# Optimization experiments

Measured on AMD Instinct MI355X. Metric: run time of the kernel, lower is better.

The kernel has to match this reference:

```python
import jax, jax.numpy as jnp
import numpy as np

NUM_CLASSES = 91
COST_CLASS, COST_BBOX, COST_GIOU = 1.0, 5.0, 2.0
W_CE, W_BBOX, W_GIOU = 2.0, 2.5, 2.0
EOS_COEF = 0.1
B, Q, T = 64, 300, 25


def box_cxcywh_to_xyxy(x):
    cx, cy, w, h = x[..., 0], x[..., 1], x[..., 2], x[..., 3]
    return jnp.stack([cx - 0.5 * w, cy - 0.5 * h, cx + 0.5 * w, cy + 0.5 * h], axis=-1)


def giou_pairwise(b1, b2):
    # b1 [N,4], b2 [M,4] in xyxy -> [N,M]
    area1 = (b1[:, 2] - b1[:, 0]) * (b1[:, 3] - b1[:, 1])
    area2 = (b2[:, 2] - b2[:, 0]) * (b2[:, 3] - b2[:, 1])
    lt = jnp.maximum(b1[:, None, :2], b2[None, :, :2])
    rb = jnp.minimum(b1[:, None, 2:], b2[None, :, 2:])
    wh = jnp.clip(rb - lt, 0.0)
    inter = wh[..., 0] * wh[..., 1]
    union = area1[:, None] + area2[None, :] - inter
    iou = inter / union
    lti = jnp.minimum(b1[:, None, :2], b2[None, :, :2])
    rbi = jnp.maximum(b1[:, None, 2:], b2[None, :, 2:])
    whi = jnp.clip(rbi - lti, 0.0)
    areai = whi[..., 0] * whi[..., 1]
    return iou - (areai - union) / areai


def giou_elementwise(b1, b2):
    # b1,b2 [N,4] xyxy -> [N]
    area1 = (b1[:, 2] - b1[:, 0]) * (b1[:, 3] - b1[:, 1])
    area2 = (b2[:, 2] - b2[:, 0]) * (b2[:, 3] - b2[:, 1])
    lt = jnp.maximum(b1[:, :2], b2[:, :2])
    rb = jnp.minimum(b1[:, 2:], b2[:, 2:])
    wh = jnp.clip(rb - lt, 0.0)
    inter = wh[:, 0] * wh[:, 1]
    union = area1 + area2 - inter
    iou = inter / union
    lti = jnp.minimum(b1[:, :2], b2[:, :2])
    rbi = jnp.maximum(b1[:, 2:], b2[:, 2:])
    whi = jnp.clip(rbi - lti, 0.0)
    areai = whi[:, 0] * whi[:, 1]
    return iou - (areai - union) / areai


def _lsa(cost):
    # Jonker-Volgenant shortest augmenting path; same optimum as scipy linear_sum_assignment
    cost = np.asarray(cost, dtype=np.float64)
    transposed = cost.shape[0] > cost.shape[1]
    if transposed:
        cost = cost.T
    n, m = cost.shape  # n <= m
    u = np.zeros(n + 1)
    v = np.zeros(m + 1)
    p = np.zeros(m + 1, dtype=np.int64)
    way = np.zeros(m + 1, dtype=np.int64)
    for i in range(1, n + 1):
        p[0] = i
        j0 = 0
        minv = np.full(m + 1, np.inf)
        used = np.zeros(m + 1, dtype=bool)
        while True:
            used[j0] = True
            i0 = p[j0]
            cur = cost[i0 - 1, :] - u[i0] - v[1:]
            free = ~used[1:]
            better = free & (cur < minv[1:])
            minv[1:][better] = cur[better]
            way[1:][better] = j0
            masked = np.where(free, minv[1:], np.inf)
            j1 = int(np.argmin(masked)) + 1
            delta = minv[j1]
            u[p[used]] += delta
            v[used] -= delta
            minv[~used] -= delta
            j0 = j1
            if p[j0] == 0:
                break
        while j0:
            j1 = way[j0]
            p[j0] = p[j1]
            j0 = j1
    rows, cols = [], []
    for j in range(1, m + 1):
        if p[j] != 0:
            rows.append(p[j] - 1)
            cols.append(j - 1)
    rows = np.asarray(rows, dtype=np.int64)
    cols = np.asarray(cols, dtype=np.int64)
    if transposed:
        rows, cols = cols, rows
    order = np.argsort(rows)
    return rows[order], cols[order]


def _match(pred_logits, pred_boxes, tgt_labels, tgt_boxes):
    # builds the full cross-batch cost matrix exactly like the torch module, then
    # solves per-image rectangular assignment on the host (non-differentiable)
    log_prob = jax.nn.log_softmax(pred_logits.reshape(B * Q, NUM_CLASSES + 1), axis=-1)
    out_bbox = pred_boxes.reshape(B * Q, 4)
    tgt_ids = tgt_labels.reshape(B * T)
    tgt_bb = tgt_boxes.reshape(B * T, 4)
    cost_class = -log_prob[:, tgt_ids]                                        # [BQ, BT]
    cost_bbox = jnp.abs(out_bbox[:, None, :] - tgt_bb[None, :, :]).sum(-1)    # L1 cdist
    cost_giou = -giou_pairwise(box_cxcywh_to_xyxy(out_bbox), box_cxcywh_to_xyxy(tgt_bb))
    C = COST_BBOX * cost_bbox + COST_CLASS * cost_class + COST_GIOU * cost_giou
    Cn = np.asarray(jax.lax.stop_gradient(C.reshape(B, Q, B * T)))
    src = np.zeros((B, T), dtype=np.int64)
    tgt = np.zeros((B, T), dtype=np.int64)
    for b in range(B):
        r, c = _lsa(Cn[b, :, b * T:(b + 1) * T])
        src[b] = r
        tgt[b] = c
    batch_idx = jnp.repeat(jnp.arange(B), T)
    return batch_idx, jnp.asarray(src.reshape(-1)), jnp.asarray(tgt.reshape(-1))


def _losses(pred_logits, pred_boxes, tgt_labels, tgt_boxes, batch_idx, src_idx, tgt_idx):
    num_t = batch_idx.shape[0]
    matched_labels = tgt_labels[batch_idx, tgt_idx]
    target_classes = jnp.full((B, Q), NUM_CLASSES, dtype=jnp.int32)
    target_classes = target_classes.at[batch_idx, src_idx].set(matched_labels)
    empty_weight = jnp.ones(NUM_CLASSES + 1, dtype=pred_logits.dtype).at[-1].set(EOS_COEF)
    logp = jax.nn.log_softmax(pred_logits, axis=-1)
    nll = -jnp.take_along_axis(logp, target_classes[..., None], axis=-1)[..., 0]
    w = empty_weight[target_classes]
    loss_ce = (w * nll).sum() / w.sum()
    src_b = pred_boxes[batch_idx, src_idx]
    tgt_b = tgt_boxes[batch_idx, tgt_idx]
    loss_bbox = jnp.abs(src_b - tgt_b).sum() / num_t
    loss_giou = (1.0 - giou_elementwise(box_cxcywh_to_xyxy(src_b), box_cxcywh_to_xyxy(tgt_b))).sum() / num_t
    l_ce = W_CE * loss_ce
    l_bb = W_BBOX * loss_bbox
    l_gi = W_GIOU * loss_giou
    return jnp.stack([l_ce, l_bb, l_gi, l_ce + l_bb + l_gi])


def setup_inputs() -> dict:
    key = jax.random.key(0)
    k1, k2, k3, k4 = jax.random.split(key, 4)
    pred_logits = jax.random.normal(k1, (B, Q, NUM_CLASSES + 1), dtype=jnp.float32)
    pred_boxes = jax.random.uniform(k2, (B, Q, 4), dtype=jnp.float32, minval=0.05, maxval=0.95)
    tgt_labels = jax.random.randint(k3, (B, T), 0, NUM_CLASSES)
    tgt_boxes = jax.random.uniform(k4, (B, T, 4), dtype=jnp.float32, minval=0.05, maxval=0.95)
    return {"pred_logits": pred_logits, "pred_boxes": pred_boxes, "tgt_labels": tgt_labels, "tgt_boxes": tgt_boxes}


def reference(pred_logits, pred_boxes, tgt_labels, tgt_boxes):
    batch_idx, src_idx, tgt_idx = _match(pred_logits, pred_boxes, tgt_labels, tgt_boxes)
    # returns [loss_ce, loss_bbox, loss_giou, loss_total] (already weight-scaled)
    return _losses(pred_logits, pred_boxes, tgt_labels, tgt_boxes, batch_idx, src_idx, tgt_idx)
```

## Files before the change

### kernel.cpp

```cpp
#include <hip/hip_runtime.h>
#include <math.h>

constexpr int B_ = 64;
constexpr int Q_ = 300;
constexpr int T_ = 25;
constexpr int NCLS = 91;
constexpr int L_ = NCLS + 1;
constexpr float C_BB = 5.0f, C_GI = 2.0f;
constexpr float W_CE = 2.0f, W_BBOX = 2.5f, W_GIOU = 2.0f;
constexpr float EOS = 0.1f;
constexpr int K_ = 5;
constexpr int TPB = 256;

__device__ __forceinline__ unsigned long long ord64(double v) {
    long long bb = __double_as_longlong(v);
    return (bb < 0) ? ~(unsigned long long)bb
                    : ((unsigned long long)bb | 0x8000000000000000ULL);
}
__device__ __forceinline__ double unord64(unsigned long long u) {
    long long bb = (u & 0x8000000000000000ULL) ? (long long)(u & 0x7FFFFFFFFFFFFFFFULL)
                                               : (long long)~u;
    return __longlong_as_double(bb);
}
__device__ __forceinline__ unsigned int ord32(float f) {
    unsigned int b = __float_as_uint(f);
    return (b & 0x80000000u) ? ~b : (b | 0x80000000u);
}
__device__ __forceinline__ unsigned long long pack14(double v, unsigned aux) {
    return (ord64(v) & ~16383ULL) | (unsigned long long)aux;
}
__device__ __forceinline__ unsigned long long pack9(double v, unsigned col) {
    return (ord64(v) & ~511ULL) | (unsigned long long)col;
}

template <int CTRL>
__device__ __forceinline__ unsigned long long dppb(unsigned long long b) {
    int lo = __builtin_amdgcn_update_dpp(0, (int)(unsigned)b, CTRL, 0xF, 0xF, true);
    int hi = __builtin_amdgcn_update_dpp(0, (int)(unsigned)(b >> 32), CTRL, 0xF, 0xF, true);
    return ((unsigned long long)(unsigned)hi << 32) | (unsigned)lo;
}
__device__ __forceinline__ unsigned long long bcast63(unsigned long long b) {
    unsigned lo = (unsigned)__builtin_amdgcn_readlane((int)(unsigned)b, 63);
    unsigned hi = (unsigned)__builtin_amdgcn_readlane((int)(unsigned)(b >> 32), 63);
    return ((unsigned long long)hi << 32) | lo;
}
__device__ __forceinline__ double readlane_f64(double v, int lane) {
    long long b = __double_as_longlong(v);
    int lo = __builtin_amdgcn_readlane((int)(unsigned)(unsigned long long)b, lane);
    int hi = __builtin_amdgcn_readlane((int)(((unsigned long long)b) >> 32), lane);
    return __longlong_as_double((long long)(((unsigned long long)(unsigned)hi << 32)
                                           | (unsigned)lo));
}

__device__ __forceinline__ unsigned long long wavemin(unsigned long long b) {
    { unsigned long long o = dppb<0xB1>(b);  if (o < b) b = o; }
    { unsigned long long o = dppb<0x4E>(b);  if (o < b) b = o; }
    { unsigned long long o = dppb<0x141>(b); if (o < b) b = o; }
    { unsigned long long o = dppb<0x140>(b); if (o < b) b = o; }
    { unsigned long long o = dppb<0x142>(b); if (o < b) b = o; }
    { unsigned long long o = dppb<0x143>(b); if (o < b) b = o; }
    return bcast63(b);
}
__device__ __forceinline__ void red2(unsigned long long& k1, unsigned long long& k2,
                                     unsigned long long o1, unsigned long long o2) {
    unsigned long long n1 = o1 < k1 ? o1 : k1;
    unsigned long long ls = o1 < k1 ? k1 : o1;
    unsigned long long n2 = k2 < o2 ? k2 : o2;
    n2 = ls < n2 ? ls : n2;
    k1 = n1; k2 = n2;
}
__device__ __forceinline__ void wavemin2(unsigned long long& k1, unsigned long long& k2) {
    red2(k1, k2, dppb<0xB1>(k1),  dppb<0xB1>(k2));
    red2(k1, k2, dppb<0x4E>(k1),  dppb<0x4E>(k2));
    red2(k1, k2, dppb<0x141>(k1), dppb<0x141>(k2));
    red2(k1, k2, dppb<0x140>(k1), dppb<0x140>(k2));
    red2(k1, k2, dppb<0x142>(k1), dppb<0x142>(k2));
    red2(k1, k2, dppb<0x143>(k1), dppb<0x143>(k2));
    k1 = bcast63(k1);
    k2 = bcast63(k2);
}

__device__ __forceinline__ float giou_f(const float px[4], float parea,
                                        const float tx[4], float tarea) {
    float ltx = fmaxf(px[0], tx[0]), lty = fmaxf(px[1], tx[1]);
    float rbx = fminf(px[2], tx[2]), rby = fminf(px[3], tx[3]);
    float iw = fmaxf(rbx - ltx, 0.f), ih = fmaxf(rby - lty, 0.f);
    float inter = iw * ih;
    float uni = parea + tarea - inter;
    float iou = inter / uni;
    float lix = fminf(px[0], tx[0]), liy = fminf(px[1], tx[1]);
    float rix = fmaxf(px[2], tx[2]), riy = fmaxf(px[3], tx[3]);
    float aw = fmaxf(rix - lix, 0.f), ah = fmaxf(riy - liy, 0.f);
    float ai = aw * ah;
    return iou - (ai - uni) / ai;
}

__global__ __launch_bounds__(TPB) void fused_kernel(
        const float* __restrict__ logits,
        const float* __restrict__ pboxes,
        const int*   __restrict__ tlabels,
        const float* __restrict__ tboxes,
        double* __restrict__ partial) {
    const int b = blockIdx.x;
    const int tid = threadIdx.x;

    __shared__ float  costL[T_][Q_];
    __shared__ float  lseL[Q_];
    __shared__ int    pL[Q_ + 1];
    __shared__ int    wayL[Q_ + 1];
    __shared__ double uL[T_ + 1];
    __shared__ double uStage[32];
    __shared__ int    argcolL[T_];
    __shared__ int    mqL[T_];
    __shared__ int    lblL[T_];
    __shared__ int    lblq[Q_];
    __shared__ float  tbL[T_][4];
    __shared__ float  txL[T_][4];
    __shared__ float  taL[T_];
    __shared__ double wsum[4][3];

    if (tid < T_) {
        lblL[tid] = tlabels[b * T_ + tid];
        mqL[tid] = 0;
        float c0 = tboxes[(size_t)(b * T_ + tid) * 4 + 0];
        float c1 = tboxes[(size_t)(b * T_ + tid) * 4 + 1];
        float c2 = tboxes[(size_t)(b * T_ + tid) * 4 + 2];
        float c3 = tboxes[(size_t)(b * T_ + tid) * 4 + 3];
        tbL[tid][0] = c0; tbL[tid][1] = c1; tbL[tid][2] = c2; tbL[tid][3] = c3;
        float x0 = c0 - 0.5f * c2, y0 = c1 - 0.5f * c3;
        float x1 = c0 + 0.5f * c2, y1 = c1 + 0.5f * c3;
        txL[tid][0] = x0; txL[tid][1] = y0; txL[tid][2] = x1; txL[tid][3] = y1;
        taL[tid] = (x1 - x0) * (y1 - y0);
    }
    for (int j = tid; j <= Q_; j += TPB) { pL[j] = 0; wayL[j] = 0; }
    for (int q = tid; q < Q_; q += TPB) lblq[q] = NCLS;
    __syncthreads();

    const float* lgb = logits + (size_t)b * Q_ * L_;
    const float* pbb = pboxes + (size_t)b * Q_ * 4;

    for (int q = tid; q < Q_; q += TPB) {
        const float4* lr4 = (const float4*)(lgb + (size_t)q * L_);
        float m0 = -INFINITY, m1 = -INFINITY, m2 = -INFINITY, m3 = -INFINITY;
        for (int c = 0; c < 23; ++c) {
            float4 v = lr4[c];
            m0 = fmaxf(m0, v.x); m1 = fmaxf(m1, v.y);
            m2 = fmaxf(m2, v.z); m3 = fmaxf(m3, v.w);
        }
        float mx = fmaxf(fmaxf(m0, m1), fmaxf(m2, m3));
        float s0 = 0.f, s1 = 0.f, s2 = 0.f, s3 = 0.f;
        for (int c = 0; c < 23; ++c) {
            float4 v = lr4[c];
            s0 += expf(v.x - mx); s1 += expf(v.y - mx);
            s2 += expf(v.z - mx); s3 += expf(v.w - mx);
        }
        float lz = mx + logf((s0 + s1) + (s2 + s3));
        lseL[q] = lz;

        float p0 = pbb[(size_t)q * 4 + 0], p1 = pbb[(size_t)q * 4 + 1];
        float p2 = pbb[(size_t)q * 4 + 2], p3 = pbb[(size_t)q * 4 + 3];
        float px[4] = { p0 - 0.5f * p2, p1 - 0.5f * p3, p0 + 0.5f * p2, p1 + 0.5f * p3 };
        float parea = (px[2] - px[0]) * (px[3] - px[1]);

#pragma unroll
        for (int t = 0; t < T_; ++t) {
            float cls = lz - lgb[(size_t)q * L_ + lblL[t]];
            float l1 = fabsf(p0 - tbL[t][0]) + fabsf(p1 - tbL[t][1]) +
                       fabsf(p2 - tbL[t][2]) + fabsf(p3 - tbL[t][3]);
            float tx[4] = { txL[t][0], txL[t][1], txL[t][2], txL[t][3] };
            float g = giou_f(px, parea, tx, taL[t]);
            costL[t][q] = C_BB * l1 + cls - C_GI * g;
        }
    }
    __syncthreads();

    {
        int w = tid >> 6, lane = tid & 63;
        for (int t = w; t < T_; t += 4) {
            unsigned long long best = ~0ULL;
#pragma unroll
            for (int k = 0; k < K_; ++k) {
                int col = lane + 64 * k;
                if (col < Q_) {
                    unsigned long long kk =
                        ((unsigned long long)ord32(costL[t][col]) << 32) | (unsigned)col;
                    if (kk < best) best = kk;
                }
            }
            best = wavemin(best);
            if (lane == 0) {
                int jc = (int)(best & 0xFFFFFFFFULL);
                argcolL[t] = jc;
                uL[t + 1] = (double)costL[t][jc];
            }
        }
    }
    __syncthreads();

    if (tid < 64) {
        int win = tid;
        if (tid < T_) {
            int myc = argcolL[tid];
            for (int j = 0; j < T_; ++j) {
                int oc = argcolL[j];
                if (oc == myc && j < win) win = j;
            }
            if (win == tid) pL[myc + 1] = tid + 1;
        }
        unsigned long long mb = __ballot(tid < T_ && win == tid);
        unsigned int freemask = (~(unsigned int)mb) & ((1u << T_) - 1);

        double v0[K_], minv[K_], stampv[K_];
        int pReg[K_];
        bool usedk[K_], validk[K_];
        double ureg = (tid >= 1 && tid <= T_) ? uL[tid] : 0.0;
#pragma unroll
        for (int k = 0; k < K_; ++k) {
            int col = tid + 64 * k;
            validk[k] = col < Q_;
            v0[k] = 0.0;
            stampv[k] = 0.0; usedk[k] = false; minv[k] = INFINITY;
            pReg[k] = validk[k] ? pL[col + 1] : 0;
        }

        for (int iter = 0; iter < 48 && freemask; ++iter) {
            int t = __builtin_ctz(freemask);
            freemask &= freemask - 1;
            const float* crow = &costL[t][0];
            unsigned long long k1 = ~0ULL, k2 = ~0ULL;
#pragma unroll
            for (int k = 0; k < K_; ++k) {
                if (validk[k]) {
                    int col = tid + 64 * k;
                    unsigned long long kk = pack9((double)crow[col] - v0[k], (unsigned)col);
                    if (kk < k1) { k2 = k1; k1 = kk; }
                    else if (kk < k2) { k2 = kk; }
                }
            }
            wavemin2(k1, k2);
            int j1 = (int)(k1 & 511ULL);
            double am1 = unord64(k1 & ~511ULL);
            double am2 = unord64(k2 & ~511ULL);
            int owner = j1 & 63, k1i = j1 >> 6;
            int psel = pReg[0];
#pragma unroll
            for (int k = 1; k < K_; ++k)
                if (k1i == k) psel = pReg[k];
            int prev = __builtin_amdgcn_readlane(psel, owner);
            if (tid == owner) {
#pragma unroll
                for (int k = 0; k < K_; ++k)
                    if (k == k1i) { v0[k] -= (am2 - am1); pReg[k] = t + 1; }
            }
            if (tid == t + 1) ureg = am2;
            if (prev) freemask |= 1u << (prev - 1);
        }

#pragma unroll
        for (int k = 0; k < K_; ++k)
            if (validk[k]) pL[tid + 1 + 64 * k] = pReg[k];

        for (int i = 1; i <= T_; ++i) {
            if (!((freemask >> (i - 1)) & 1u)) continue;
            if (tid == 0) pL[0] = i;
#pragma unroll
            for (int k = 0; k < K_; ++k) { minv[k] = INFINITY; usedk[k] = false; }
            double S = 0.0;
            int j0 = 0, i0 = i;
            double u0i0 = readlane_f64(ureg, i);

            for (int step = 0; step < 512; ++step) {
                double a = u0i0 - S;
                const float* crow = &costL[i0 - 1][0];
                unsigned long long bk = ~0ULL;
#pragma unroll
                for (int k = 0; k < K_; ++k) {
                    if (validk[k] && !usedk[k]) {
                        int col = tid + 64 * k;
                        double cur = (double)crow[col] - a - v0[k];
                        if (cur < minv[k]) { minv[k] = cur; wayL[col + 1] = j0; }
                        unsigned long long kk = pack14(
                            minv[k], ((unsigned)(col + 1) << 5) | (unsigned)pReg[k]);
                        if (kk < bk) bk = kk;
                    }
                }
                bk = wavemin(bk);
                int j1  = (int)((bk >> 5) & 511ULL);
                int i0n = (int)(bk & 31ULL);
                double Snew = unord64(bk & ~16383ULL);
                S = Snew;
                j0 = j1;
                if (i0n == 0) break;
                int owner = (j1 - 1) & 63, k1i = (j1 - 1) >> 6;
                if (tid == owner) {
#pragma unroll
                    for (int k = 0; k < K_; ++k)
                        if (k == k1i) { usedk[k] = true; stampv[k] = Snew; }
                }
                i0 = i0n;
                u0i0 = readlane_f64(ureg, i0);
            }

            if (tid <= T_) uStage[tid] = 0.0;
#pragma unroll
            for (int k = 0; k < K_; ++k) {
                if (validk[k] && usedk[k]) {
                    double d = S - stampv[k];
                    v0[k] -= d;
                    uStage[pReg[k]] = d;
                }
            }
            if (tid >= 1 && tid <= T_) ureg += uStage[tid];
            if (tid == i) ureg += S;
            if (tid == 0) {
                int jj = j0;
                while (jj) { int jn = wayL[jj]; pL[jj] = pL[jn]; jj = jn; }
            }
#pragma unroll
            for (int k = 0; k < K_; ++k)
                if (validk[k]) pReg[k] = pL[tid + 1 + 64 * k];
        }

#pragma unroll
        for (int k = 0; k < K_; ++k)
            if (validk[k] && pReg[k] > 0) mqL[pReg[k] - 1] = tid + 64 * k;
        if (tid < T_) lblq[mqL[tid]] = lblL[tid];
    }
    __syncthreads();

    double ce = 0.0, sb = 0.0, sg = 0.0;
    for (int q = tid; q < Q_; q += TPB) {
        int label = lblq[q];
        float nll = lseL[q] - lgb[(size_t)q * L_ + label];
        float w = (label == NCLS) ? EOS : 1.0f;
        ce += (double)(w * nll);
    }
    if (tid < T_) {
        int q = mqL[tid];
        float p0 = pbb[(size_t)q * 4 + 0], p1 = pbb[(size_t)q * 4 + 1];
        float p2 = pbb[(size_t)q * 4 + 2], p3 = pbb[(size_t)q * 4 + 3];
        sb = (double)(fabsf(p0 - tbL[tid][0]) + fabsf(p1 - tbL[tid][1]) +
                      fabsf(p2 - tbL[tid][2]) + fabsf(p3 - tbL[tid][3]));
        float px[4] = { p0 - 0.5f * p2, p1 - 0.5f * p3, p0 + 0.5f * p2, p1 + 0.5f * p3 };
        float parea = (px[2] - px[0]) * (px[3] - px[1]);
        float tx[4] = { txL[tid][0], txL[tid][1], txL[tid][2], txL[tid][3] };
        float g = giou_f(px, parea, tx, taL[tid]);
        sg = (double)(1.0f - g);
    }
#pragma unroll
    for (int off = 1; off < 64; off <<= 1) {
        ce += __shfl_xor(ce, off);
        sb += __shfl_xor(sb, off);
        sg += __shfl_xor(sg, off);
    }
    if ((tid & 63) == 0) {
        int w = tid >> 6;
        wsum[w][0] = ce; wsum[w][1] = sb; wsum[w][2] = sg;
    }
    __syncthreads();
    if (tid == 0) {
        double a0 = 0, a1 = 0, a2 = 0;
        for (int w = 0; w < 4; ++w) { a0 += wsum[w][0]; a1 += wsum[w][1]; a2 += wsum[w][2]; }
        partial[(size_t)b * 3 + 0] = a0;
        partial[(size_t)b * 3 + 1] = a1;
        partial[(size_t)b * 3 + 2] = a2;
    }
}

__global__ __launch_bounds__(64) void finalize_kernel(const double* __restrict__ partial,
                                                      float* __restrict__ out) {
    int tid = threadIdx.x;
    double a = partial[(size_t)tid * 3 + 0];
    double c = partial[(size_t)tid * 3 + 1];
    double g = partial[(size_t)tid * 3 + 2];
#pragma unroll
    for (int off = 1; off < 64; off <<= 1) {
        a += __shfl_xor(a, off);
        c += __shfl_xor(c, off);
        g += __shfl_xor(g, off);
    }
    if (tid == 0) {
        float lce = W_CE * (float)(a / 3360.0);
        float lbb = W_BBOX * (float)(c / 1600.0);
        float lgi = W_GIOU * (float)(g / 1600.0);
        out[0] = lce;
        out[1] = lbb;
        out[2] = lgi;
        out[3] = lce + lbb + lgi;
    }
}

extern "C" void kernel_launch(void* const* d_in, const int* in_sizes, int n_in,
                              void* d_out, int out_size, void* d_ws, size_t ws_size,
                              hipStream_t stream) {
    (void)in_sizes; (void)n_in; (void)out_size; (void)ws_size;
    const float* logits  = (const float*)d_in[0];
    const float* pboxes  = (const float*)d_in[1];
    const int*   tlabels = (const int*)d_in[2];
    const float* tboxes  = (const float*)d_in[3];
    float* out = (float*)d_out;
    double* partial = (double*)d_ws;

    fused_kernel<<<B_, TPB, 0, stream>>>(logits, pboxes, tlabels, tboxes, partial);
    finalize_kernel<<<1, 64, 0, stream>>>(partial, out);
}
```

Baseline: 36.47 us.

## Pair two free rows per auction step and fuse finalize via atomic last-block reduction

The auction-style initial assignment loop now processes two free target rows per iteration, scanning both cost rows together and running an interleaved double wave-min reduction. This is meant to halve the serial iteration count and hide reduction latency. On a column conflict the second row is returned to the free mask. Separately, the finalize kernel is replaced by atomic accumulation with a last-block counter, plus a memset. This trades a second kernel launch for a memset node and atomics, and makes the floating-point summation order nondeterministic.

```diff
diff --git a/kernel.cpp b/kernel.cpp
--- a/kernel.cpp
+++ b/kernel.cpp
@@ -78,6 +78,23 @@
     red2(k1, k2, dppb<0x143>(k1), dppb<0x143>(k2));
     k1 = bcast63(k1);
     k2 = bcast63(k2);
+}
+__device__ __forceinline__ void wavemin2x2(unsigned long long& a1, unsigned long long& a2,
+                                           unsigned long long& b1, unsigned long long& b2) {
+    red2(a1, a2, dppb<0xB1>(a1),  dppb<0xB1>(a2));
+    red2(b1, b2, dppb<0xB1>(b1),  dppb<0xB1>(b2));
+    red2(a1, a2, dppb<0x4E>(a1),  dppb<0x4E>(a2));
+    red2(b1, b2, dppb<0x4E>(b1),  dppb<0x4E>(b2));
+    red2(a1, a2, dppb<0x141>(a1), dppb<0x141>(a2));
+    red2(b1, b2, dppb<0x141>(b1), dppb<0x141>(b2));
+    red2(a1, a2, dppb<0x140>(a1), dppb<0x140>(a2));
+    red2(b1, b2, dppb<0x140>(b1), dppb<0x140>(b2));
+    red2(a1, a2, dppb<0x142>(a1), dppb<0x142>(a2));
+    red2(b1, b2, dppb<0x142>(b1), dppb<0x142>(b2));
+    red2(a1, a2, dppb<0x143>(a1), dppb<0x143>(a2));
+    red2(b1, b2, dppb<0x143>(b1), dppb<0x143>(b2));
+    a1 = bcast63(a1); a2 = bcast63(a2);
+    b1 = bcast63(b1); b2 = bcast63(b2);
 }
 
 __device__ __forceinline__ float giou_f(const float px[4], float parea,
@@ -100,7 +117,8 @@
         const float* __restrict__ pboxes,
         const int*   __restrict__ tlabels,
         const float* __restrict__ tboxes,
-        double* __restrict__ partial) {
+        double* acc,
+        float* out) {
     const int b = blockIdx.x;
     const int tid = threadIdx.x;
 
@@ -224,36 +242,68 @@
         }
 
         for (int iter = 0; iter < 48 && freemask; ++iter) {
-            int t = __builtin_ctz(freemask);
+            int t1 = __builtin_ctz(freemask);
             freemask &= freemask - 1;
-            const float* crow = &costL[t][0];
-            unsigned long long k1 = ~0ULL, k2 = ~0ULL;
+            int t2 = freemask ? __builtin_ctz(freemask) : -1;
+            if (t2 >= 0) freemask &= freemask - 1;
+
+            const float* crow1 = &costL[t1][0];
+            const float* crow2 = &costL[(t2 >= 0 ? t2 : t1)][0];
+            unsigned long long a1 = ~0ULL, a2 = ~0ULL, b1 = ~0ULL, b2 = ~0ULL;
 #pragma unroll
             for (int k = 0; k < K_; ++k) {
                 if (validk[k]) {
                     int col = tid + 64 * k;
-                    unsigned long long kk = pack9((double)crow[col] - v0[k], (unsigned)col);
-                    if (kk < k1) { k2 = k1; k1 = kk; }
-                    else if (kk < k2) { k2 = kk; }
-                }
-            }
-            wavemin2(k1, k2);
-            int j1 = (int)(k1 & 511ULL);
-            double am1 = unord64(k1 & ~511ULL);
-            double am2 = unord64(k2 & ~511ULL);
-            int owner = j1 & 63, k1i = j1 >> 6;
-            int psel = pReg[0];
-#pragma unroll
-            for (int k = 1; k < K_; ++k)
-                if (k1i == k) psel = pReg[k];
-            int prev = __builtin_amdgcn_readlane(psel, owner);
-            if (tid == owner) {
+                    double base = v0[k];
+                    unsigned long long ka = pack9((double)crow1[col] - base, (unsigned)col);
+                    if (ka < a1) { a2 = a1; a1 = ka; } else if (ka < a2) { a2 = ka; }
+                    unsigned long long kb = pack9((double)crow2[col] - base, (unsigned)col);
+                    if (kb < b1) { b2 = b1; b1 = kb; } else if (kb < b2) { b2 = kb; }
+                }
+            }
+            wavemin2x2(a1, a2, b1, b2);
+
+            int j1 = (int)(a1 & 511ULL);
+            double am1 = unord64(a1 & ~511ULL);
+            double am2 = unord64(a2 & ~511ULL);
+            int owner1 = j1 & 63, k1i = j1 >> 6;
+            int j2 = (t2 >= 0) ? (int)(b1 & 511ULL) : -1;
+            int owner2 = (j2 >= 0) ? (j2 & 63) : 0;
+            int k2i = (j2 >= 0) ? (j2 >> 6) : 0;
+
+            int psel1 = pReg[0], psel2 = pReg[0];
+#pragma unroll
+            for (int k = 1; k < K_; ++k) {
+                if (k1i == k) psel1 = pReg[k];
+                if (k2i == k) psel2 = pReg[k];
+            }
+            int prev1 = __builtin_amdgcn_readlane(psel1, owner1);
+            int prev2 = (j2 >= 0 && j2 != j1)
+                        ? __builtin_amdgcn_readlane(psel2, owner2) : 0;
+
+            if (tid == owner1) {
 #pragma unroll
                 for (int k = 0; k < K_; ++k)
-                    if (k == k1i) { v0[k] -= (am2 - am1); pReg[k] = t + 1; }
-            }
-            if (tid == t + 1) ureg = am2;
-            if (prev) freemask |= 1u << (prev - 1);
+                    if (k == k1i) { v0[k] -= (am2 - am1); pReg[k] = t1 + 1; }
+            }
+            if (tid == t1 + 1) ureg = am2;
+            if (prev1) freemask |= 1u << (prev1 - 1);
+
+            if (t2 >= 0) {
+                if (j2 != j1) {
+                    double bm1 = unord64(b1 & ~511ULL);
+                    double bm2 = unord64(b2 & ~511ULL);
+                    if (tid == owner2) {
+#pragma unroll
+                        for (int k = 0; k < K_; ++k)
+                            if (k == k2i) { v0[k] -= (bm2 - bm1); pReg[k] = t2 + 1; }
+                    }
+                    if (tid == t2 + 1) ureg = bm2;
+                    if (prev2) freemask |= 1u << (prev2 - 1);
+                } else {
+                    freemask |= 1u << t2;
+                }
+            }
         }
 
 #pragma unroll
@@ -358,35 +408,29 @@
         wsum[w][0] = ce; wsum[w][1] = sb; wsum[w][2] = sg;
     }
     __syncthreads();
+
     if (tid == 0) {
         double a0 = 0, a1 = 0, a2 = 0;
         for (int w = 0; w < 4; ++w) { a0 += wsum[w][0]; a1 += wsum[w][1]; a2 += wsum[w][2]; }
-        partial[(size_t)b * 3 + 0] = a0;
-        partial[(size_t)b * 3 + 1] = a1;
-        partial[(size_t)b * 3 + 2] = a2;
-    }
-}
-
-__global__ __launch_bounds__(64) void finalize_kernel(const double* __restrict__ partial,
-                                                      float* __restrict__ out) {
-    int tid = threadIdx.x;
-    double a = partial[(size_t)tid * 3 + 0];
-    double c = partial[(size_t)tid * 3 + 1];
-    double g = partial[(size_t)tid * 3 + 2];
-#pragma unroll
-    for (int off = 1; off < 64; off <<= 1) {
-        a += __shfl_xor(a, off);
-        c += __shfl_xor(c, off);
-        g += __shfl_xor(g, off);
-    }
-    if (tid == 0) {
-        float lce = W_CE * (float)(a / 3360.0);
-        float lbb = W_BBOX * (float)(c / 1600.0);
-        float lgi = W_GIOU * (float)(g / 1600.0);
-        out[0] = lce;
-        out[1] = lbb;
-        out[2] = lgi;
-        out[3] = lce + lbb + lgi;
+        atomicAdd(&acc[0], a0);
+        atomicAdd(&acc[1], a1);
+        atomicAdd(&acc[2], a2);
+        __threadfence();
+        unsigned* cnt = (unsigned*)(acc + 3);
+        unsigned old = atomicAdd(cnt, 1u);
+        if (old == (unsigned)(B_ - 1)) {
+            __threadfence();
+            double A = atomicAdd(&acc[0], 0.0);
+            double C = atomicAdd(&acc[1], 0.0);
+            double G = atomicAdd(&acc[2], 0.0);
+            float lce = W_CE * (float)(A / 3360.0);
+            float lbb = W_BBOX * (float)(C / 1600.0);
+            float lgi = W_GIOU * (float)(G / 1600.0);
+            out[0] = lce;
+            out[1] = lbb;
+            out[2] = lgi;
+            out[3] = lce + lbb + lgi;
+        }
     }
 }
 
@@ -399,8 +443,8 @@
     const int*   tlabels = (const int*)d_in[2];
     const float* tboxes  = (const float*)d_in[3];
     float* out = (float*)d_out;
-    double* partial = (double*)d_ws;
-
-    fused_kernel<<<B_, TPB, 0, stream>>>(logits, pboxes, tlabels, tboxes, partial);
-    finalize_kernel<<<1, 64, 0, stream>>>(partial, out);
-}
+    double* acc = (double*)d_ws;
+
+    hipMemsetAsync(d_ws, 0, 64, stream);
+    fused_kernel<<<B_, TPB, 0, stream>>>(logits, pboxes, tlabels, tboxes, acc, out);
+}
```

Measured after the change: 43.46 us. 1.19x slower.
